# Kernel optimization log

Measured on AMD Instinct MI355X. Metric: run time of the kernel, lower is better.

The kernel has to match this reference:

```python
import jax, jax.numpy as jnp
import numpy as np

N = 200000
W = 255  # hidden width hard-coded in the module


def _linear_params(key, fan_in, fan_out, w_std=0.02, b_val=0.0):
    kw, _ = jax.random.split(key)
    w = jax.random.normal(kw, (fan_in, fan_out), dtype=jnp.float32) * w_std
    b = jnp.full((fan_out,), b_val, dtype=jnp.float32)
    return w, b


def setup_inputs() -> dict:
    key = jax.random.key(0)
    ks = jax.random.split(key, 20)
    inp = {
        "opacity_emb": jax.random.normal(ks[0], (N, 1), dtype=jnp.float32),
        "shs_emb": jax.random.normal(ks[1], (N, 16, 3), dtype=jnp.float32),
        "time_emb": jax.random.uniform(ks[2], (N, 1), dtype=jnp.float32),
        "semantic_feature": jax.random.normal(ks[3], (N, 128), dtype=jnp.float32),
        "point": jax.random.normal(ks[4], (N, 3), dtype=jnp.float32),
        "scales_input": jax.random.normal(ks[5], (N, 3), dtype=jnp.float32),
        "rotations_input": jax.random.normal(ks[6], (N, 4), dtype=jnp.float32),
        "dx": jax.random.normal(ks[7], (N, 3), dtype=jnp.float32),
    }
    # mask_net: ReLU -> Linear(W,W) -> ReLU -> Linear(W,1) -> sigmoid
    inp["mask_w1"], inp["mask_b1"] = _linear_params(ks[8], W, W)
    inp["mask_w2"], inp["mask_b2"] = _linear_params(ks[9], W, 1)
    # deform heads: ReLU -> Linear(W,W) -> ReLU -> Linear(W,out)
    inp["pos_w1"], inp["pos_b1"] = _linear_params(ks[10], W, W)
    inp["pos_w2"], inp["pos_b2"] = _linear_params(ks[11], W, 3)
    inp["scl_w1"], inp["scl_b1"] = _linear_params(ks[12], W, W)
    inp["scl_w2"], inp["scl_b2"] = _linear_params(ks[13], W, 3)
    inp["rot_w1"], inp["rot_b1"] = _linear_params(ks[14], W, W)
    inp["rot_w2"], inp["rot_b2"] = _linear_params(ks[15], W, 4)
    inp["shs_w1"], inp["shs_b1"] = _linear_params(ks[16], W, W)
    inp["shs_w2"], inp["shs_b2"] = _linear_params(ks[17], W, 48)
    return inp


def _head(hidden, w1, b1, w2, b2):
    # ReLU -> Linear -> ReLU -> Linear (matches nn.Sequential in the module)
    h = jax.nn.relu(hidden)
    h = jax.nn.relu(h @ w1 + b1)
    return h @ w2 + b2


def _time_pos_enc(time_emb, n):
    # vectorized version of the scalar sin/cos for-loop: uses only time_emb[0, 0]
    t = time_emb[0, 0]
    i = jnp.arange(0, 64, 2, dtype=jnp.float32)          # even indices
    freq = jnp.power(jnp.float32(10000.0), i / jnp.float32(32.0))  # 10000**(2*i/64)
    enc = jnp.stack([jnp.sin(t / freq), jnp.cos(t / freq)], axis=1).reshape(64)
    return jnp.broadcast_to(enc[None, :], (n, 64))


def reference(opacity_emb, shs_emb, time_emb, semantic_feature, point,
              scales_input, rotations_input, dx,
              mask_w1, mask_b1, mask_w2, mask_b2,
              pos_w1, pos_b1, pos_w2, pos_b2,
              scl_w1, scl_b1, scl_w2, scl_b2,
              rot_w1, rot_b1, rot_w2, rot_b2,
              shs_w1, shs_b1, shs_w2, shs_b2):
    n = shs_emb.shape[0]
    shs_flat = shs_emb.reshape(n, 48)
    tpe = _time_pos_enc(time_emb, n)                     # [N, 64]
    hidden = jnp.concatenate(
        (point, rotations_input, scales_input, opacity_emb,
         shs_flat, semantic_feature, dx, time_emb, tpe), axis=1)  # [N, 255]

    mask = jax.nn.sigmoid(_head(hidden, mask_w1, mask_b1, mask_w2, mask_b2))  # [N, 1]

    dx_out = _head(hidden, pos_w1, pos_b1, pos_w2, pos_b2)        # [N, 3]
    pts = point + dx_out * mask

    ds = _head(hidden, scl_w1, scl_b1, scl_w2, scl_b2)            # [N, 3]
    scales = scales_input + ds * mask

    dr = _head(hidden, rot_w1, rot_b1, rot_w2, rot_b2)            # [N, 4]
    rotations = rotations_input + dr * mask

    opacity = opacity_emb[:, :1]

    dshs = _head(hidden, shs_w1, shs_b1, shs_w2, shs_b2).reshape(n, 16, 3)
    shs = shs_emb + dshs * mask[:, :, None]

    return (pts, scales, rotations, opacity, shs, dx_out, dshs)
```

## Files before the change

### kernel.cpp

```cpp
#include <hip/hip_runtime.h>
#include <math.h>

typedef unsigned short u16;
typedef __attribute__((ext_vector_type(8))) short short8;
typedef __attribute__((ext_vector_type(4))) float floatx4;

__device__ __forceinline__ u16 f2bf(float f) {
    union { float f; unsigned u; } v; v.f = f;
    unsigned r = v.u + 0x7fffu + ((v.u >> 16) & 1u);
    return (u16)(r >> 16);
}

struct WPtrs {
    const float* w1[5];
    const float* w2[5];
    const float* b1[5];
};

typedef const __attribute__((address_space(1))) unsigned GUA;
typedef __attribute__((address_space(3))) unsigned LUA;

__device__ __forceinline__ void stage24(const u16* gbase, u16* lbase, int wave, int lane) {
    const char* g = (const char*)gbase;
    char* l = (char*)lbase;
#pragma unroll
    for (int i = 0; i < 6; ++i) {
        int off = (wave * 6 + i) * 1024;
        __builtin_amdgcn_global_load_lds((GUA*)(g + off + lane * 16), (LUA*)(l + off), 16, 0, 0);
    }
}

__global__ void prep_weights(WPtrs p, const float* __restrict__ te,
                             u16* __restrict__ W1t, u16* __restrict__ W2t,
                             float* __restrict__ W2f, float* __restrict__ b1eff)
{
    const int bid = blockIdx.x;
    const int tid = threadIdx.x;
    if (bid < 60) {
        __shared__ float tile[64 * 65];
        int h = bid / 12, t = bid % 12;
        int k0 = (t / 4) * 64, n0 = (t % 4) * 64;
        int nn = tid & 63, g = tid >> 6;
        const float* w1 = p.w1[h];
#pragma unroll
        for (int rep = 0; rep < 16; ++rep) {
            int kl = g * 16 + rep;
            int k = k0 + kl, nidx = n0 + nn;
            float v = (k < 191 && nidx < 255) ? w1[k * 255 + nidx] : 0.0f;
            tile[kl * 65 + nn] = v;
        }
        __syncthreads();
#pragma unroll
        for (int i = 0; i < 2; ++i) {
            int c = tid * 2 + i;
            int nl = c >> 3, kcl = c & 7;
            int n = n0 + nl;
            int kcg = (k0 >> 3) + kcl;
            short8 sv;
#pragma unroll
            for (int j = 0; j < 8; ++j)
                sv[j] = (short)f2bf(tile[(kcl * 8 + j) * 65 + nl]);
            *(short8*)(W1t + h * 49152 + n * 192 + ((kcg ^ (n & 7)) << 3)) = sv;
        }
    } else if (bid < 172) {
        int row = bid - 60;
        int h, roff, od;
        if (row < 16)      { h = 0; roff = 0;  od = 1; }
        else if (row < 32) { h = 1; roff = 16; od = 3; }
        else if (row < 48) { h = 2; roff = 32; od = 3; }
        else if (row < 64) { h = 3; roff = 48; od = 4; }
        else               { h = 4; roff = 64; od = 48; }
        int n2 = row - roff;
        int k = tid;
        float v = (k < 255 && n2 < od) ? p.w2[h][k * od + n2] : 0.0f;
        W2t[row * 256 + k] = f2bf(v);
        if (h < 4 && n2 < od) {
            int r11b = (h == 0) ? 0 : (h == 1) ? 1 : (h == 2) ? 4 : 7;
            W2f[(r11b + n2) * 256 + k] = v;
        }
    } else {
        __shared__ float encL[64];
        if (tid < 64) {
            float t = te[0];
            float fi = (float)(tid & ~1);
            float freq = powf(10000.0f, fi * (1.0f / 32.0f));
            float a = t / freq;
            float v = (tid & 1) ? cosf(a) : sinf(a);
            encL[tid] = fmaxf(v, 0.0f);
        }
        __syncthreads();
        for (int e = tid; e < 5 * 256; e += 256) {
            int h = e >> 8, col = e & 255;
            float s = 0.0f;
            if (col < 255) {
                s = p.b1[h][col];
                const float* w1 = p.w1[h];
#pragma unroll 8
                for (int j = 0; j < 64; ++j)
                    s += w1[(191 + j) * 255 + col] * encL[j];
            }
            b1eff[h * 256 + col] = s;
        }
    }
}

struct FusedArgs {
    const u16* W1t; const u16* W2t; const float* W2f; const float* b1eff;
    const float* b2[5];
    const float* opa; const float* shs; const float* te; const float* sem;
    const float* pt;  const float* scl; const float* rot; const float* dxp;
    float* out; int n;
};

__device__ __forceinline__ short8 gather8(const FusedArgs& A, int row, int c0)
{
    short8 sv;
    if (c0 >= 64 && c0 <= 176) {
        const float* s = A.sem + (size_t)row * 128 + (c0 - 59);
        float4 a = *(const float4*)(s);
        float4 b = *(const float4*)(s + 4);
        sv[0] = (short)f2bf(fmaxf(a.x, 0.f)); sv[1] = (short)f2bf(fmaxf(a.y, 0.f));
        sv[2] = (short)f2bf(fmaxf(a.z, 0.f)); sv[3] = (short)f2bf(fmaxf(a.w, 0.f));
        sv[4] = (short)f2bf(fmaxf(b.x, 0.f)); sv[5] = (short)f2bf(fmaxf(b.y, 0.f));
        sv[6] = (short)f2bf(fmaxf(b.z, 0.f)); sv[7] = (short)f2bf(fmaxf(b.w, 0.f));
    } else {
#pragma unroll
        for (int j = 0; j < 8; ++j) {
            int c = c0 + j;
            float v;
            if (c < 3)        v = A.pt[row * 3 + c];
            else if (c < 7)   v = A.rot[row * 4 + (c - 3)];
            else if (c < 10)  v = A.scl[row * 3 + (c - 7)];
            else if (c < 11)  v = A.opa[row];
            else if (c < 59)  v = A.shs[(size_t)row * 48 + (c - 11)];
            else if (c < 187) v = A.sem[(size_t)row * 128 + (c - 59)];
            else if (c < 190) v = A.dxp[row * 3 + (c - 187)];
            else if (c < 191) v = A.te[row];
            else              v = 0.0f;
            sv[j] = (short)f2bf(fmaxf(v, 0.0f));
        }
    }
    return sv;
}

__global__ __launch_bounds__(256, 3) void fused_all(FusedArgs A)
{
    __shared__ u16 W1L[2][12288];

    const int tid = threadIdx.x;
    const int wave = tid >> 6;
    const int lane = tid & 63;
    const int q = lane >> 4, ln = lane & 15;
    const int n = A.n;
    const size_t NN = (size_t)n;

    stage24(A.W1t, W1L[0], wave, lane);

    const int r0 = blockIdx.x * 128 + wave * 32;
    const int ra0 = min(r0 + ln, n - 1);
    const int ra1 = min(r0 + 16 + ln, n - 1);
    const int g0 = r0 + ln, g1 = r0 + 16 + ln;

    short8 xf[2][6];
#pragma unroll
    for (int kk = 0; kk < 6; ++kk) {
        int c0 = kk * 32 + q * 8;
        xf[0][kk] = gather8(A, ra0, c0);
        xf[1][kk] = gather8(A, ra1, c0);
    }

    __syncthreads();

    floatx4 acc[4][2];
    floatx4 acc2[3][2];
    float out2[4][2];
    float mkb0 = 0.f, mkb1 = 0.f;

#pragma unroll 1
    for (int c = 0; c < 20; ++c) {
        const int h = c >> 2;
        const int Q = c & 3;
        if (c + 1 < 20)
            stage24(A.W1t + (c + 1) * 12288, W1L[(c + 1) & 1], wave, lane);
        const u16* buf = W1L[c & 1];

#pragma unroll
        for (int ct = 0; ct < 4; ++ct) {
            acc[ct][0] = (floatx4){0.f, 0.f, 0.f, 0.f};
            acc[ct][1] = (floatx4){0.f, 0.f, 0.f, 0.f};
        }
#pragma unroll
        for (int kk = 0; kk < 6; ++kk) {
#pragma unroll
            for (int ct = 0; ct < 4; ++ct) {
                int nl = ct * 16 + ln;
                int sw = (kk * 4 + q) ^ (ln & 7);
                short8 wf = *(const short8*)(buf + nl * 192 + (sw << 3));
                acc[ct][0] = __builtin_amdgcn_mfma_f32_16x16x32_bf16(wf, xf[0][kk], acc[ct][0], 0, 0, 0);
                acc[ct][1] = __builtin_amdgcn_mfma_f32_16x16x32_bf16(wf, xf[1][kk], acc[ct][1], 0, 0, 0);
            }
        }

#pragma unroll
        for (int ct = 0; ct < 4; ++ct) {
            floatx4 b4 = *(const floatx4*)(A.b1eff + h * 256 + Q * 64 + ct * 16 + q * 4);
#pragma unroll
            for (int t = 0; t < 2; ++t) {
                floatx4 v = acc[ct][t];
                v.x = fmaxf(v.x + b4.x, 0.f);
                v.y = fmaxf(v.y + b4.y, 0.f);
                v.z = fmaxf(v.z + b4.z, 0.f);
                v.w = fmaxf(v.w + b4.w, 0.f);
                acc[ct][t] = v;
            }
        }

        if (h < 4) {
            const int od = (h == 0) ? 1 : (h == 3) ? 4 : 3;
            const int r11b = (h == 0) ? 0 : (h == 1) ? 1 : (h == 2) ? 4 : 7;
            if (Q == 0) {
#pragma unroll
                for (int m = 0; m < 4; ++m) { out2[m][0] = 0.f; out2[m][1] = 0.f; }
            }
            const float* wb = A.W2f + r11b * 256 + Q * 64 + q * 4;
#pragma unroll
            for (int n2 = 0; n2 < 4; ++n2) {
                if (n2 < od) {
#pragma unroll
                    for (int ct = 0; ct < 4; ++ct) {
                        floatx4 w4 = *(const floatx4*)(wb + n2 * 256 + ct * 16);
#pragma unroll
                        for (int t = 0; t < 2; ++t) {
                            out2[n2][t] = fmaf(acc[ct][t].x, w4.x, out2[n2][t]);
                            out2[n2][t] = fmaf(acc[ct][t].y, w4.y, out2[n2][t]);
                            out2[n2][t] = fmaf(acc[ct][t].z, w4.z, out2[n2][t]);
                            out2[n2][t] = fmaf(acc[ct][t].w, w4.w, out2[n2][t]);
                        }
                    }
                }
            }
            if (Q == 3) {
#pragma unroll
                for (int n2 = 0; n2 < 4; ++n2) {
#pragma unroll
                    for (int t = 0; t < 2; ++t) {
                        float v = out2[n2][t];
                        v += __shfl_xor(v, 16, 64);
                        v += __shfl_xor(v, 32, 64);
                        out2[n2][t] = v;
                    }
                }
                const float* b2h = A.b2[h];
                if (h == 0) {
                    mkb0 = 1.0f / (1.0f + expf(-(out2[0][0] + b2h[0])));
                    mkb1 = 1.0f / (1.0f + expf(-(out2[0][1] + b2h[0])));
                    if (q == 0) {
                        if (g0 < n) A.out[10 * NN + g0] = A.opa[g0];
                        if (g1 < n) A.out[10 * NN + g1] = A.opa[g1];
                    }
                } else if (q == 0) {
#pragma unroll
                    for (int t = 0; t < 2; ++t) {
                        int grow = t ? g1 : g0;
                        float mk = t ? mkb1 : mkb0;
                        if (grow < n) {
                            if (h == 1) {
#pragma unroll
                                for (int r = 0; r < 3; ++r) {
                                    float raw = out2[r][t] + b2h[r];
                                    A.out[59 * NN + (size_t)grow * 3 + r] = raw;
                                    A.out[(size_t)grow * 3 + r] = A.pt[(size_t)grow * 3 + r] + raw * mk;
                                }
                            } else if (h == 2) {
#pragma unroll
                                for (int r = 0; r < 3; ++r) {
                                    float raw = out2[r][t] + b2h[r];
                                    A.out[3 * NN + (size_t)grow * 3 + r] = A.scl[(size_t)grow * 3 + r] + raw * mk;
                                }
                            } else {
#pragma unroll
                                for (int r = 0; r < 4; ++r) {
                                    float raw = out2[r][t] + b2h[r];
                                    A.out[6 * NN + (size_t)grow * 4 + r] = A.rot[(size_t)grow * 4 + r] + raw * mk;
                                }
                            }
                        }
                    }
                }
            }
        } else {
            if (Q == 0) {
#pragma unroll
                for (int mt = 0; mt < 3; ++mt) {
                    acc2[mt][0] = (floatx4){0.f, 0.f, 0.f, 0.f};
                    acc2[mt][1] = (floatx4){0.f, 0.f, 0.f, 0.f};
                }
            }
            const u16* w2th = A.W2t + 64 * 256;
#pragma unroll
            for (int ks = 0; ks < 2; ++ks) {
                int ksg = Q * 2 + ks;
                short8 a2[3];
#pragma unroll
                for (int mt = 0; mt < 3; ++mt)
                    a2[mt] = *(const short8*)(w2th + (mt * 16 + ln) * 256 + ksg * 32 + q * 8);
#pragma unroll
                for (int t = 0; t < 2; ++t) {
                    short8 bfrag;
#pragma unroll
                    for (int j = 0; j < 8; ++j) {
                        int idx = (((q * 2 + (j >> 2)) & 3) << 4) | ln;
                        float v0 = __shfl(acc[ks * 2 + 0][t][j & 3], idx, 64);
                        float v1 = __shfl(acc[ks * 2 + 1][t][j & 3], idx, 64);
                        bfrag[j] = (short)f2bf((q >> 1) ? v1 : v0);
                    }
#pragma unroll
                    for (int mt = 0; mt < 3; ++mt)
                        acc2[mt][t] = __builtin_amdgcn_mfma_f32_16x16x32_bf16(a2[mt], bfrag, acc2[mt][t], 0, 0, 0);
                }
            }
            if (Q == 3) {
                const float* b2h = A.b2[4];
#pragma unroll
                for (int t = 0; t < 2; ++t) {
                    int grow = t ? g1 : g0;
                    float mk = t ? mkb1 : mkb0;
                    if (grow < n) {
#pragma unroll
                        for (int mt = 0; mt < 3; ++mt) {
                            int n2b = mt * 16 + q * 4;
                            floatx4 b2v = *(const floatx4*)(b2h + n2b);
                            floatx4 raw = acc2[mt][t] + b2v;
                            *(floatx4*)(A.out + 62 * NN + (size_t)grow * 48 + n2b) = raw;
                            floatx4 s = *(const floatx4*)(A.shs + (size_t)grow * 48 + n2b);
                            *(floatx4*)(A.out + 11 * NN + (size_t)grow * 48 + n2b) = s + raw * mk;
                        }
                    }
                }
            }
        }

        __syncthreads();
    }
}

extern "C" void kernel_launch(void* const* d_in, const int* in_sizes, int n_in,
                              void* d_out, int out_size, void* d_ws, size_t ws_size,
                              hipStream_t stream)
{
    const float* opa  = (const float*)d_in[0];
    const float* shs  = (const float*)d_in[1];
    const float* te   = (const float*)d_in[2];
    const float* sem  = (const float*)d_in[3];
    const float* pt   = (const float*)d_in[4];
    const float* scl  = (const float*)d_in[5];
    const float* rot  = (const float*)d_in[6];
    const float* dx   = (const float*)d_in[7];

    WPtrs p;
    p.w1[0] = (const float*)d_in[8];  p.w2[0] = (const float*)d_in[10]; p.b1[0] = (const float*)d_in[9];
    p.w1[1] = (const float*)d_in[12]; p.w2[1] = (const float*)d_in[14]; p.b1[1] = (const float*)d_in[13];
    p.w1[2] = (const float*)d_in[16]; p.w2[2] = (const float*)d_in[18]; p.b1[2] = (const float*)d_in[17];
    p.w1[3] = (const float*)d_in[20]; p.w2[3] = (const float*)d_in[22]; p.b1[3] = (const float*)d_in[21];
    p.w1[4] = (const float*)d_in[24]; p.w2[4] = (const float*)d_in[26]; p.b1[4] = (const float*)d_in[25];

    const int n = in_sizes[0];

    char* ws = (char*)d_ws;
    u16*   W1t   = (u16*)ws;
    u16*   W2t   = (u16*)(ws + 491520);
    float* W2f   = (float*)(ws + 491520 + 57344);
    float* b1eff = (float*)(ws + 491520 + 57344 + 11264);

    prep_weights<<<173, 256, 0, stream>>>(p, te, W1t, W2t, W2f, b1eff);

    FusedArgs A;
    A.W1t = W1t; A.W2t = W2t; A.W2f = W2f; A.b1eff = b1eff;
    A.b2[0] = (const float*)d_in[11];
    A.b2[1] = (const float*)d_in[15];
    A.b2[2] = (const float*)d_in[19];
    A.b2[3] = (const float*)d_in[23];
    A.b2[4] = (const float*)d_in[27];
    A.opa = opa; A.shs = shs; A.te = te; A.sem = sem;
    A.pt = pt; A.scl = scl; A.rot = rot; A.dxp = dx;
    A.out = (float*)d_out; A.n = n;

    int grid = (n + 127) / 128;
    fused_all<<<grid, 256, 0, stream>>>(A);
}
```

Measured before the change: 534.4 us.

## Unroll chunk loop into templated quarters and repack small-head output weights

Replaces the 20-iteration runtime chunk loop with an outer loop over heads that calls a template instantiated per quarter. Buffer parity and the Q==0/Q==3 branches become compile-time constants, and the swizzled LDS offsets are precomputed once per thread. Small-head second-layer weights are repacked into an interleaved [k][4] float layout, so each float4 load supplies all outputs for one k, accumulated in an acc2 register instead of the separate out2 array. The weight prep also spreads the bias-fold step over 5 blocks with shared-memory tiles, in exchange for larger code size and possibly different register allocation.

```diff
diff --git a/kernel.cpp b/kernel.cpp
--- a/kernel.cpp
+++ b/kernel.cpp
@@ -32,7 +32,7 @@
 
 __global__ void prep_weights(WPtrs p, const float* __restrict__ te,
                              u16* __restrict__ W1t, u16* __restrict__ W2t,
-                             float* __restrict__ W2f, float* __restrict__ b1eff)
+                             float* __restrict__ W2ft4, float* __restrict__ b1eff)
 {
     const int bid = blockIdx.x;
     const int tid = threadIdx.x;
@@ -74,12 +74,21 @@
         int k = tid;
         float v = (k < 255 && n2 < od) ? p.w2[h][k * od + n2] : 0.0f;
         W2t[row * 256 + k] = f2bf(v);
-        if (h < 4 && n2 < od) {
-            int r11b = (h == 0) ? 0 : (h == 1) ? 1 : (h == 2) ? 4 : 7;
-            W2f[(r11b + n2) * 256 + k] = v;
+    } else if (bid < 176) {
+        int h = bid - 172;
+        const int od = (h == 0) ? 1 : (h == 3) ? 4 : 3;
+        int k = tid;
+#pragma unroll
+        for (int n2 = 0; n2 < 4; ++n2) {
+            float v = (k < 255 && n2 < od) ? p.w2[h][k * od + n2] : 0.0f;
+            W2ft4[h * 1024 + k * 4 + n2] = v;
         }
     } else {
+        int h = bid - 176;
+        __shared__ float wtail[64 * 255];
         __shared__ float encL[64];
+        const float* wt = p.w1[h] + 191 * 255;
+        for (int i = tid; i < 64 * 255; i += 256) wtail[i] = wt[i];
         if (tid < 64) {
             float t = te[0];
             float fi = (float)(tid & ~1);
@@ -89,23 +98,20 @@
             encL[tid] = fmaxf(v, 0.0f);
         }
         __syncthreads();
-        for (int e = tid; e < 5 * 256; e += 256) {
-            int h = e >> 8, col = e & 255;
-            float s = 0.0f;
-            if (col < 255) {
-                s = p.b1[h][col];
-                const float* w1 = p.w1[h];
+        int col = tid;
+        float s = 0.0f;
+        if (col < 255) {
+            s = p.b1[h][col];
 #pragma unroll 8
-                for (int j = 0; j < 64; ++j)
-                    s += w1[(191 + j) * 255 + col] * encL[j];
-            }
-            b1eff[h * 256 + col] = s;
-        }
+            for (int j = 0; j < 64; ++j)
+                s += wtail[j * 255 + col] * encL[j];
+        }
+        b1eff[h * 256 + col] = s;
     }
 }
 
 struct FusedArgs {
-    const u16* W1t; const u16* W2t; const float* W2f; const float* b1eff;
+    const u16* W1t; const u16* W2t; const float* W2ft4; const float* b1eff;
     const float* b2[5];
     const float* opa; const float* shs; const float* te; const float* sem;
     const float* pt;  const float* scl; const float* rot; const float* dxp;
@@ -143,6 +149,175 @@
     return sv;
 }
 
+template<int Q>
+__device__ __forceinline__ void quarter(const FusedArgs& A, int h, u16* bufs,
+                                        int wave, int lane, int q, int ln,
+                                        const int (&bofs)[6],
+                                        const short8 (&xf)[2][6],
+                                        floatx4 (&acc2)[3][2],
+                                        float& mkb0, float& mkb1,
+                                        int g0, int g1)
+{
+    const int n = A.n;
+    const size_t NN = (size_t)n;
+
+    const int chunk = h * 4 + Q + 1;
+    if (chunk < 20)
+        stage24(A.W1t + chunk * 12288, bufs + ((Q + 1) & 1) * 12288, wave, lane);
+
+    floatx4 acc[4][2];
+#pragma unroll
+    for (int ct = 0; ct < 4; ++ct) {
+        acc[ct][0] = (floatx4){0.f, 0.f, 0.f, 0.f};
+        acc[ct][1] = (floatx4){0.f, 0.f, 0.f, 0.f};
+    }
+    const char* bb = (const char*)bufs + (Q & 1) * 24576;
+#pragma unroll
+    for (int kk = 0; kk < 6; ++kk) {
+#pragma unroll
+        for (int ct = 0; ct < 4; ++ct) {
+            short8 wf = *(const short8*)(bb + bofs[kk] + ct * 6144);
+            acc[ct][0] = __builtin_amdgcn_mfma_f32_16x16x32_bf16(wf, xf[0][kk], acc[ct][0], 0, 0, 0);
+            acc[ct][1] = __builtin_amdgcn_mfma_f32_16x16x32_bf16(wf, xf[1][kk], acc[ct][1], 0, 0, 0);
+        }
+    }
+
+#pragma unroll
+    for (int ct = 0; ct < 4; ++ct) {
+        floatx4 b4 = *(const floatx4*)(A.b1eff + h * 256 + Q * 64 + ct * 16 + q * 4);
+#pragma unroll
+        for (int t = 0; t < 2; ++t) {
+            floatx4 v = acc[ct][t];
+            v.x = fmaxf(v.x + b4.x, 0.f);
+            v.y = fmaxf(v.y + b4.y, 0.f);
+            v.z = fmaxf(v.z + b4.z, 0.f);
+            v.w = fmaxf(v.w + b4.w, 0.f);
+            acc[ct][t] = v;
+        }
+    }
+
+    if (Q == 0) {
+#pragma unroll
+        for (int mt = 0; mt < 3; ++mt) {
+            acc2[mt][0] = (floatx4){0.f, 0.f, 0.f, 0.f};
+            acc2[mt][1] = (floatx4){0.f, 0.f, 0.f, 0.f};
+        }
+    }
+
+    if (h < 4) {
+        const float* w4p = A.W2ft4 + h * 1024 + (Q * 64 + q * 4) * 4;
+#pragma unroll
+        for (int ct = 0; ct < 4; ++ct) {
+#pragma unroll
+            for (int comp = 0; comp < 4; ++comp) {
+                floatx4 wv = *(const floatx4*)(w4p + ct * 64 + comp * 4);
+#pragma unroll
+                for (int t = 0; t < 2; ++t) {
+                    float a = acc[ct][t][comp];
+                    acc2[0][t].x = fmaf(a, wv.x, acc2[0][t].x);
+                    acc2[0][t].y = fmaf(a, wv.y, acc2[0][t].y);
+                    acc2[0][t].z = fmaf(a, wv.z, acc2[0][t].z);
+                    acc2[0][t].w = fmaf(a, wv.w, acc2[0][t].w);
+                }
+            }
+        }
+        if (Q == 3) {
+#pragma unroll
+            for (int t = 0; t < 2; ++t) {
+#pragma unroll
+                for (int r = 0; r < 4; ++r) {
+                    float v = acc2[0][t][r];
+                    v += __shfl_xor(v, 16, 64);
+                    v += __shfl_xor(v, 32, 64);
+                    acc2[0][t][r] = v;
+                }
+            }
+            const float* b2h = A.b2[h];
+            if (h == 0) {
+                mkb0 = 1.0f / (1.0f + expf(-(acc2[0][0][0] + b2h[0])));
+                mkb1 = 1.0f / (1.0f + expf(-(acc2[0][1][0] + b2h[0])));
+                if (q == 0) {
+                    if (g0 < n) A.out[10 * NN + g0] = A.opa[g0];
+                    if (g1 < n) A.out[10 * NN + g1] = A.opa[g1];
+                }
+            } else if (q == 0) {
+#pragma unroll
+                for (int t = 0; t < 2; ++t) {
+                    int grow = t ? g1 : g0;
+                    float mk = t ? mkb1 : mkb0;
+                    if (grow < n) {
+                        if (h == 1) {
+#pragma unroll
+                            for (int r = 0; r < 3; ++r) {
+                                float raw = acc2[0][t][r] + b2h[r];
+                                A.out[59 * NN + (size_t)grow * 3 + r] = raw;
+                                A.out[(size_t)grow * 3 + r] = A.pt[(size_t)grow * 3 + r] + raw * mk;
+                            }
+                        } else if (h == 2) {
+#pragma unroll
+                            for (int r = 0; r < 3; ++r) {
+                                float raw = acc2[0][t][r] + b2h[r];
+                                A.out[3 * NN + (size_t)grow * 3 + r] = A.scl[(size_t)grow * 3 + r] + raw * mk;
+                            }
+                        } else {
+#pragma unroll
+                            for (int r = 0; r < 4; ++r) {
+                                float raw = acc2[0][t][r] + b2h[r];
+                                A.out[6 * NN + (size_t)grow * 4 + r] = A.rot[(size_t)grow * 4 + r] + raw * mk;
+                            }
+                        }
+                    }
+                }
+            }
+        }
+    } else {
+        const u16* w2th = A.W2t + 64 * 256;
+#pragma unroll
+        for (int ks = 0; ks < 2; ++ks) {
+            const int ksg = Q * 2 + ks;
+            short8 a2[3];
+#pragma unroll
+            for (int mt = 0; mt < 3; ++mt)
+                a2[mt] = *(const short8*)(w2th + (mt * 16 + ln) * 256 + ksg * 32 + q * 8);
+#pragma unroll
+            for (int t = 0; t < 2; ++t) {
+                short8 bfrag;
+#pragma unroll
+                for (int j = 0; j < 8; ++j) {
+                    int idx = (((q * 2 + (j >> 2)) & 3) << 4) | ln;
+                    float v0 = __shfl(acc[ks * 2 + 0][t][j & 3], idx, 64);
+                    float v1 = __shfl(acc[ks * 2 + 1][t][j & 3], idx, 64);
+                    bfrag[j] = (short)f2bf((q >> 1) ? v1 : v0);
+                }
+#pragma unroll
+                for (int mt = 0; mt < 3; ++mt)
+                    acc2[mt][t] = __builtin_amdgcn_mfma_f32_16x16x32_bf16(a2[mt], bfrag, acc2[mt][t], 0, 0, 0);
+            }
+        }
+        if (Q == 3) {
+            const float* b2h = A.b2[4];
+#pragma unroll
+            for (int t = 0; t < 2; ++t) {
+                int grow = t ? g1 : g0;
+                float mk = t ? mkb1 : mkb0;
+                if (grow < n) {
+#pragma unroll
+                    for (int mt = 0; mt < 3; ++mt) {
+                        int n2b = mt * 16 + q * 4;
+                        floatx4 b2v = *(const floatx4*)(b2h + n2b);
+                        floatx4 raw = acc2[mt][t] + b2v;
+                        *(floatx4*)(A.out + 62 * NN + (size_t)grow * 48 + n2b) = raw;
+                        floatx4 s = *(const floatx4*)(A.shs + (size_t)grow * 48 + n2b);
+                        *(floatx4*)(A.out + 11 * NN + (size_t)grow * 48 + n2b) = s + raw * mk;
+                    }
+                }
+            }
+        }
+    }
+
+    __syncthreads();
+}
+
 __global__ __launch_bounds__(256, 3) void fused_all(FusedArgs A)
 {
     __shared__ u16 W1L[2][12288];
@@ -152,9 +327,9 @@
     const int lane = tid & 63;
     const int q = lane >> 4, ln = lane & 15;
     const int n = A.n;
-    const size_t NN = (size_t)n;
-
-    stage24(A.W1t, W1L[0], wave, lane);
+    u16* bufs = &W1L[0][0];
+
+    stage24(A.W1t, bufs, wave, lane);
 
     const int r0 = blockIdx.x * 128 + wave * 32;
     const int ra0 = min(r0 + ln, n - 1);
@@ -169,178 +344,22 @@
         xf[1][kk] = gather8(A, ra1, c0);
     }
 
+    int bofs[6];
+#pragma unroll
+    for (int kk = 0; kk < 6; ++kk)
+        bofs[kk] = ln * 384 + ((((kk * 4 + q) ^ (ln & 7))) << 4);
+
     __syncthreads();
 
-    floatx4 acc[4][2];
     floatx4 acc2[3][2];
-    float out2[4][2];
     float mkb0 = 0.f, mkb1 = 0.f;
 
 #pragma unroll 1
-    for (int c = 0; c < 20; ++c) {
-        const int h = c >> 2;
-        const int Q = c & 3;
-        if (c + 1 < 20)
-            stage24(A.W1t + (c + 1) * 12288, W1L[(c + 1) & 1], wave, lane);
-        const u16* buf = W1L[c & 1];
-
-#pragma unroll
-        for (int ct = 0; ct < 4; ++ct) {
-            acc[ct][0] = (floatx4){0.f, 0.f, 0.f, 0.f};
-            acc[ct][1] = (floatx4){0.f, 0.f, 0.f, 0.f};
-        }
-#pragma unroll
-        for (int kk = 0; kk < 6; ++kk) {
-#pragma unroll
-            for (int ct = 0; ct < 4; ++ct) {
-                int nl = ct * 16 + ln;
-                int sw = (kk * 4 + q) ^ (ln & 7);
-                short8 wf = *(const short8*)(buf + nl * 192 + (sw << 3));
-                acc[ct][0] = __builtin_amdgcn_mfma_f32_16x16x32_bf16(wf, xf[0][kk], acc[ct][0], 0, 0, 0);
-                acc[ct][1] = __builtin_amdgcn_mfma_f32_16x16x32_bf16(wf, xf[1][kk], acc[ct][1], 0, 0, 0);
-            }
-        }
-
-#pragma unroll
-        for (int ct = 0; ct < 4; ++ct) {
-            floatx4 b4 = *(const floatx4*)(A.b1eff + h * 256 + Q * 64 + ct * 16 + q * 4);
-#pragma unroll
-            for (int t = 0; t < 2; ++t) {
-                floatx4 v = acc[ct][t];
-                v.x = fmaxf(v.x + b4.x, 0.f);
-                v.y = fmaxf(v.y + b4.y, 0.f);
-                v.z = fmaxf(v.z + b4.z, 0.f);
-                v.w = fmaxf(v.w + b4.w, 0.f);
-                acc[ct][t] = v;
-            }
-        }
-
-        if (h < 4) {
-            const int od = (h == 0) ? 1 : (h == 3) ? 4 : 3;
-            const int r11b = (h == 0) ? 0 : (h == 1) ? 1 : (h == 2) ? 4 : 7;
-            if (Q == 0) {
-#pragma unroll
-                for (int m = 0; m < 4; ++m) { out2[m][0] = 0.f; out2[m][1] = 0.f; }
-            }
-            const float* wb = A.W2f + r11b * 256 + Q * 64 + q * 4;
-#pragma unroll
-            for (int n2 = 0; n2 < 4; ++n2) {
-                if (n2 < od) {
-#pragma unroll
-                    for (int ct = 0; ct < 4; ++ct) {
-                        floatx4 w4 = *(const floatx4*)(wb + n2 * 256 + ct * 16);
-#pragma unroll
-                        for (int t = 0; t < 2; ++t) {
-                            out2[n2][t] = fmaf(acc[ct][t].x, w4.x, out2[n2][t]);
-                            out2[n2][t] = fmaf(acc[ct][t].y, w4.y, out2[n2][t]);
-                            out2[n2][t] = fmaf(acc[ct][t].z, w4.z, out2[n2][t]);
-                            out2[n2][t] = fmaf(acc[ct][t].w, w4.w, out2[n2][t]);
-                        }
-                    }
-                }
-            }
-            if (Q == 3) {
-#pragma unroll
-                for (int n2 = 0; n2 < 4; ++n2) {
-#pragma unroll
-                    for (int t = 0; t < 2; ++t) {
-                        float v = out2[n2][t];
-                        v += __shfl_xor(v, 16, 64);
-                        v += __shfl_xor(v, 32, 64);
-                        out2[n2][t] = v;
-                    }
-                }
-                const float* b2h = A.b2[h];
-                if (h == 0) {
-                    mkb0 = 1.0f / (1.0f + expf(-(out2[0][0] + b2h[0])));
-                    mkb1 = 1.0f / (1.0f + expf(-(out2[0][1] + b2h[0])));
-                    if (q == 0) {
-                        if (g0 < n) A.out[10 * NN + g0] = A.opa[g0];
-                        if (g1 < n) A.out[10 * NN + g1] = A.opa[g1];
-                    }
-                } else if (q == 0) {
-#pragma unroll
-                    for (int t = 0; t < 2; ++t) {
-                        int grow = t ? g1 : g0;
-                        float mk = t ? mkb1 : mkb0;
-                        if (grow < n) {
-                            if (h == 1) {
-#pragma unroll
-                                for (int r = 0; r < 3; ++r) {
-                                    float raw = out2[r][t] + b2h[r];
-                                    A.out[59 * NN + (size_t)grow * 3 + r] = raw;
-                                    A.out[(size_t)grow * 3 + r] = A.pt[(size_t)grow * 3 + r] + raw * mk;
-                                }
-                            } else if (h == 2) {
-#pragma unroll
-                                for (int r = 0; r < 3; ++r) {
-                                    float raw = out2[r][t] + b2h[r];
-                                    A.out[3 * NN + (size_t)grow * 3 + r] = A.scl[(size_t)grow * 3 + r] + raw * mk;
-                                }
-                            } else {
-#pragma unroll
-                                for (int r = 0; r < 4; ++r) {
-                                    float raw = out2[r][t] + b2h[r];
-                                    A.out[6 * NN + (size_t)grow * 4 + r] = A.rot[(size_t)grow * 4 + r] + raw * mk;
-                                }
-                            }
-                        }
-                    }
-                }
-            }
-        } else {
-            if (Q == 0) {
-#pragma unroll
-                for (int mt = 0; mt < 3; ++mt) {
-                    acc2[mt][0] = (floatx4){0.f, 0.f, 0.f, 0.f};
-                    acc2[mt][1] = (floatx4){0.f, 0.f, 0.f, 0.f};
-                }
-            }
-            const u16* w2th = A.W2t + 64 * 256;
-#pragma unroll
-            for (int ks = 0; ks < 2; ++ks) {
-                int ksg = Q * 2 + ks;
-                short8 a2[3];
-#pragma unroll
-                for (int mt = 0; mt < 3; ++mt)
-                    a2[mt] = *(const short8*)(w2th + (mt * 16 + ln) * 256 + ksg * 32 + q * 8);
-#pragma unroll
-                for (int t = 0; t < 2; ++t) {
-                    short8 bfrag;
-#pragma unroll
-                    for (int j = 0; j < 8; ++j) {
-                        int idx = (((q * 2 + (j >> 2)) & 3) << 4) | ln;
-                        float v0 = __shfl(acc[ks * 2 + 0][t][j & 3], idx, 64);
-                        float v1 = __shfl(acc[ks * 2 + 1][t][j & 3], idx, 64);
-                        bfrag[j] = (short)f2bf((q >> 1) ? v1 : v0);
-                    }
-#pragma unroll
-                    for (int mt = 0; mt < 3; ++mt)
-                        acc2[mt][t] = __builtin_amdgcn_mfma_f32_16x16x32_bf16(a2[mt], bfrag, acc2[mt][t], 0, 0, 0);
-                }
-            }
-            if (Q == 3) {
-                const float* b2h = A.b2[4];
-#pragma unroll
-                for (int t = 0; t < 2; ++t) {
-                    int grow = t ? g1 : g0;
-                    float mk = t ? mkb1 : mkb0;
-                    if (grow < n) {
-#pragma unroll
-                        for (int mt = 0; mt < 3; ++mt) {
-                            int n2b = mt * 16 + q * 4;
-                            floatx4 b2v = *(const floatx4*)(b2h + n2b);
-                            floatx4 raw = acc2[mt][t] + b2v;
-                            *(floatx4*)(A.out + 62 * NN + (size_t)grow * 48 + n2b) = raw;
-                            floatx4 s = *(const floatx4*)(A.shs + (size_t)grow * 48 + n2b);
-                            *(floatx4*)(A.out + 11 * NN + (size_t)grow * 48 + n2b) = s + raw * mk;
-                        }
-                    }
-                }
-            }
-        }
-
-        __syncthreads();
+    for (int h = 0; h < 5; ++h) {
+        quarter<0>(A, h, bufs, wave, lane, q, ln, bofs, xf, acc2, mkb0, mkb1, g0, g1);
+        quarter<1>(A, h, bufs, wave, lane, q, ln, bofs, xf, acc2, mkb0, mkb1, g0, g1);
+        quarter<2>(A, h, bufs, wave, lane, q, ln, bofs, xf, acc2, mkb0, mkb1, g0, g1);
+        quarter<3>(A, h, bufs, wave, lane, q, ln, bofs, xf, acc2, mkb0, mkb1, g0, g1);
     }
 }
 
@@ -369,13 +388,13 @@
     char* ws = (char*)d_ws;
     u16*   W1t   = (u16*)ws;
     u16*   W2t   = (u16*)(ws + 491520);
-    float* W2f   = (float*)(ws + 491520 + 57344);
-    float* b1eff = (float*)(ws + 491520 + 57344 + 11264);
-
-    prep_weights<<<173, 256, 0, stream>>>(p, te, W1t, W2t, W2f, b1eff);
+    float* W2ft4 = (float*)(ws + 491520 + 57344);
+    float* b1eff = (float*)(ws + 491520 + 57344 + 16384);
+
+    prep_weights<<<181, 256, 0, stream>>>(p, te, W1t, W2t, W2ft4, b1eff);
 
     FusedArgs A;
-    A.W1t = W1t; A.W2t = W2t; A.W2f = W2f; A.b1eff = b1eff;
+    A.W1t = W1t; A.W2t = W2t; A.W2ft4 = W2ft4; A.b1eff = b1eff;
     A.b2[0] = (const float*)d_in[11];
     A.b2[1] = (const float*)d_in[15];
     A.b2[2] = (const float*)d_in[19];
```

Result: slower. 606.6 us (+13.5%).

## Halve weight chunks, triple-buffer LDS with one barrier per step, raise occupancy

Applied to the files above, without the earlier changes.

The fused MLP kernel now streams first-layer weights in 32-column chunks instead of 64, across 40 iterations with a three-slot LDS ring. The next-but-one chunk is prefetched, and each step uses a single explicit s_waitcnt plus barrier instead of two __syncthreads. Shared memory per block drops from 48 KB to 36 KB and launch bounds ask for 4 blocks per CU, aiming for more latency hiding and less barrier stall. In exchange there are twice as many loop iterations and barriers. The hand-written vmcnt count also ties correctness to the exact number of outstanding loads.

```diff
diff --git a/kernel.cpp b/kernel.cpp
--- a/kernel.cpp
+++ b/kernel.cpp
@@ -20,12 +20,12 @@
 typedef const __attribute__((address_space(1))) unsigned GUA;
 typedef __attribute__((address_space(3))) unsigned LUA;
 
-__device__ __forceinline__ void stage24(const u16* gbase, u16* lbase, int wave, int lane) {
+__device__ __forceinline__ void stage12(const u16* gbase, u16* lbase, int wave, int lane) {
     const char* g = (const char*)gbase;
     char* l = (char*)lbase;
 #pragma unroll
-    for (int i = 0; i < 6; ++i) {
-        int off = (wave * 6 + i) * 1024;
+    for (int i = 0; i < 3; ++i) {
+        int off = (wave * 3 + i) * 1024;
         __builtin_amdgcn_global_load_lds((GUA*)(g + off + lane * 16), (LUA*)(l + off), 16, 0, 0);
     }
 }
@@ -143,9 +143,9 @@
     return sv;
 }
 
-__global__ __launch_bounds__(256, 3) void fused_all(FusedArgs A)
+__global__ __launch_bounds__(256, 4) void fused_all(FusedArgs A)
 {
-    __shared__ u16 W1L[2][12288];
+    __shared__ u16 W1L[3][6144];
 
     const int tid = threadIdx.x;
     const int wave = tid >> 6;
@@ -154,7 +154,7 @@
     const int n = A.n;
     const size_t NN = (size_t)n;
 
-    stage24(A.W1t, W1L[0], wave, lane);
+    stage12(A.W1t, W1L[0], wave, lane);
 
     const int r0 = blockIdx.x * 128 + wave * 32;
     const int ra0 = min(r0 + ln, n - 1);
@@ -169,30 +169,36 @@
         xf[1][kk] = gather8(A, ra1, c0);
     }
 
-    __syncthreads();
-
-    floatx4 acc[4][2];
+    stage12(A.W1t + 6144, W1L[1], wave, lane);
+
+    floatx4 acc[2][2];
     floatx4 acc2[3][2];
     float out2[4][2];
     float mkb0 = 0.f, mkb1 = 0.f;
 
 #pragma unroll 1
-    for (int c = 0; c < 20; ++c) {
-        const int h = c >> 2;
-        const int Q = c & 3;
-        if (c + 1 < 20)
-            stage24(A.W1t + (c + 1) * 12288, W1L[(c + 1) & 1], wave, lane);
-        const u16* buf = W1L[c & 1];
-
-#pragma unroll
-        for (int ct = 0; ct < 4; ++ct) {
+    for (int c = 0; c < 40; ++c) {
+        const int h = c >> 3;
+        const int oct = c & 7;
+
+        if (c == 39) asm volatile("s_waitcnt vmcnt(0) lgkmcnt(0)" ::: "memory");
+        else         asm volatile("s_waitcnt vmcnt(3) lgkmcnt(0)" ::: "memory");
+        __builtin_amdgcn_s_barrier();
+
+        if (c + 2 < 40)
+            stage12(A.W1t + (size_t)(c + 2) * 6144, W1L[(c + 2) % 3], wave, lane);
+
+        const u16* buf = W1L[c % 3];
+
+#pragma unroll
+        for (int ct = 0; ct < 2; ++ct) {
             acc[ct][0] = (floatx4){0.f, 0.f, 0.f, 0.f};
             acc[ct][1] = (floatx4){0.f, 0.f, 0.f, 0.f};
         }
 #pragma unroll
         for (int kk = 0; kk < 6; ++kk) {
 #pragma unroll
-            for (int ct = 0; ct < 4; ++ct) {
+            for (int ct = 0; ct < 2; ++ct) {
                 int nl = ct * 16 + ln;
                 int sw = (kk * 4 + q) ^ (ln & 7);
                 short8 wf = *(const short8*)(buf + nl * 192 + (sw << 3));
@@ -202,8 +208,8 @@
         }
 
 #pragma unroll
-        for (int ct = 0; ct < 4; ++ct) {
-            floatx4 b4 = *(const floatx4*)(A.b1eff + h * 256 + Q * 64 + ct * 16 + q * 4);
+        for (int ct = 0; ct < 2; ++ct) {
+            floatx4 b4 = *(const floatx4*)(A.b1eff + h * 256 + oct * 32 + ct * 16 + q * 4);
 #pragma unroll
             for (int t = 0; t < 2; ++t) {
                 floatx4 v = acc[ct][t];
@@ -218,16 +224,16 @@
         if (h < 4) {
             const int od = (h == 0) ? 1 : (h == 3) ? 4 : 3;
             const int r11b = (h == 0) ? 0 : (h == 1) ? 1 : (h == 2) ? 4 : 7;
-            if (Q == 0) {
+            if (oct == 0) {
 #pragma unroll
                 for (int m = 0; m < 4; ++m) { out2[m][0] = 0.f; out2[m][1] = 0.f; }
             }
-            const float* wb = A.W2f + r11b * 256 + Q * 64 + q * 4;
+            const float* wb = A.W2f + r11b * 256 + oct * 32 + q * 4;
 #pragma unroll
             for (int n2 = 0; n2 < 4; ++n2) {
                 if (n2 < od) {
 #pragma unroll
-                    for (int ct = 0; ct < 4; ++ct) {
+                    for (int ct = 0; ct < 2; ++ct) {
                         floatx4 w4 = *(const floatx4*)(wb + n2 * 256 + ct * 16);
 #pragma unroll
                         for (int t = 0; t < 2; ++t) {
@@ -239,7 +245,7 @@
                     }
                 }
             }
-            if (Q == 3) {
+            if (oct == 7) {
 #pragma unroll
                 for (int n2 = 0; n2 < 4; ++n2) {
 #pragma unroll
@@ -289,7 +295,7 @@
                 }
             }
         } else {
-            if (Q == 0) {
+            if (oct == 0) {
 #pragma unroll
                 for (int mt = 0; mt < 3; ++mt) {
                     acc2[mt][0] = (floatx4){0.f, 0.f, 0.f, 0.f};
@@ -297,29 +303,25 @@
                 }
             }
             const u16* w2th = A.W2t + 64 * 256;
-#pragma unroll
-            for (int ks = 0; ks < 2; ++ks) {
-                int ksg = Q * 2 + ks;
-                short8 a2[3];
+            short8 a2[3];
+#pragma unroll
+            for (int mt = 0; mt < 3; ++mt)
+                a2[mt] = *(const short8*)(w2th + (mt * 16 + ln) * 256 + oct * 32 + q * 8);
+#pragma unroll
+            for (int t = 0; t < 2; ++t) {
+                short8 bfrag;
+#pragma unroll
+                for (int j = 0; j < 8; ++j) {
+                    int idx = (((q * 2 + (j >> 2)) & 3) << 4) | ln;
+                    float v0 = __shfl(acc[0][t][j & 3], idx, 64);
+                    float v1 = __shfl(acc[1][t][j & 3], idx, 64);
+                    bfrag[j] = (short)f2bf((q >> 1) ? v1 : v0);
+                }
 #pragma unroll
                 for (int mt = 0; mt < 3; ++mt)
-                    a2[mt] = *(const short8*)(w2th + (mt * 16 + ln) * 256 + ksg * 32 + q * 8);
-#pragma unroll
-                for (int t = 0; t < 2; ++t) {
-                    short8 bfrag;
-#pragma unroll
-                    for (int j = 0; j < 8; ++j) {
-                        int idx = (((q * 2 + (j >> 2)) & 3) << 4) | ln;
-                        float v0 = __shfl(acc[ks * 2 + 0][t][j & 3], idx, 64);
-                        float v1 = __shfl(acc[ks * 2 + 1][t][j & 3], idx, 64);
-                        bfrag[j] = (short)f2bf((q >> 1) ? v1 : v0);
-                    }
-#pragma unroll
-                    for (int mt = 0; mt < 3; ++mt)
-                        acc2[mt][t] = __builtin_amdgcn_mfma_f32_16x16x32_bf16(a2[mt], bfrag, acc2[mt][t], 0, 0, 0);
-                }
-            }
-            if (Q == 3) {
+                    acc2[mt][t] = __builtin_amdgcn_mfma_f32_16x16x32_bf16(a2[mt], bfrag, acc2[mt][t], 0, 0, 0);
+            }
+            if (oct == 7) {
                 const float* b2h = A.b2[4];
 #pragma unroll
                 for (int t = 0; t < 2; ++t) {
@@ -339,8 +341,6 @@
                 }
             }
         }
-
-        __syncthreads();
     }
 }
 
```

Result: slower. 586.4 us (+9.7%).
